# Kernel optimization log

Hardware: AMD Instinct MI355X
Metric: run time of the kernel (lower is better)

The kernel has to match this reference:

```python
import jax, jax.numpy as jnp
import numpy as np

N_HEADS = 16
MAX_CACHE_LEN = 8192
LN_EPS = 1e-5


def _layernorm(x, g, b):
    mu = jnp.mean(x, axis=-1, keepdims=True)
    var = jnp.var(x, axis=-1, keepdims=True)
    return (x - mu) * jax.lax.rsqrt(var + LN_EPS) * g + b


def setup_inputs() -> dict:
    key = jax.random.key(0)
    ks = jax.random.split(key, 8)
    b, t, d, latdim, past = 2, 2048, 2048, 512, 2048
    s = 0.02
    return {
        "x": jax.random.normal(ks[0], (b, t, d), jnp.float32),
        "latent_prev": jax.random.normal(ks[1], (b, past, latdim), jnp.float32),
        "Wq": jax.random.normal(ks[2], (d, d), jnp.float32) * s,
        "Wdown": jax.random.normal(ks[3], (d, latdim), jnp.float32) * s,
        "Wk_up": jax.random.normal(ks[4], (latdim, d), jnp.float32) * s,
        "Wv_up": jax.random.normal(ks[5], (latdim, d), jnp.float32) * s,
        "ln_g": jnp.ones((latdim,), jnp.float32),
        "ln_b": jnp.zeros((latdim,), jnp.float32),
        "Wo": jax.random.normal(ks[6], (d, d), jnp.float32) * s,
    }


def reference(x, latent_prev, Wq, Wdown, Wk_up, Wv_up, ln_g, ln_b, Wo):
    b, t, d = x.shape
    H = N_HEADS
    hd = d // H
    # q projection -> [b, t, H, hd]
    q = (x @ Wq).reshape(b, t, H, hd)
    # latent down-projection + LayerNorm, concat with cache, trim to max_cache_len
    latent_new = _layernorm(x @ Wdown, ln_g, ln_b)
    latent = jnp.concatenate([latent_prev, latent_new], axis=1)
    latent = latent[:, -MAX_CACHE_LEN:]
    S = latent.shape[1]
    past_len = min(latent_prev.shape[1], S - t)
    # up-project K/V from latent -> [b, S, H, hd]
    k = (latent @ Wk_up).reshape(b, S, H, hd)
    v = (latent @ Wv_up).reshape(b, S, H, hd)
    # offset-causal SDPA: query i attends keys j <= past_len + i
    scores = jnp.einsum("bthd,bshd->bhts", q, k) / jnp.sqrt(jnp.asarray(hd, x.dtype))
    i = jnp.arange(t)[:, None]
    j = jnp.arange(S)[None, :]
    mask = j <= (past_len + i)  # [t, S]
    scores = jnp.where(mask[None, None], scores, jnp.asarray(-1e30, scores.dtype))
    attn = jax.nn.softmax(scores, axis=-1)
    out = jnp.einsum("bhts,bshd->bthd", attn, v).reshape(b, t, d)
    return out @ Wo
```

## Files before the change

### kernel.cpp

```cpp
#include <hip/hip_runtime.h>
#include <hip/hip_bf16.h>

using bf16_t = __bf16;
typedef __bf16 bf16x8 __attribute__((ext_vector_type(8)));
typedef __bf16 bf16x4 __attribute__((ext_vector_type(4)));
typedef __bf16 bf16x2 __attribute__((ext_vector_type(2)));
typedef float  f32x4  __attribute__((ext_vector_type(4)));
typedef float  f32x16 __attribute__((ext_vector_type(16)));
typedef unsigned u32x4 __attribute__((ext_vector_type(4)));

#define MFMA16(a,b,c) __builtin_amdgcn_mfma_f32_16x16x32_bf16((a),(b),(c),0,0,0)
#define MFMA32(a,b,c) __builtin_amdgcn_mfma_f32_32x32x16_bf16((a),(b),(c),0,0,0)

__device__ __forceinline__ void load_lds16(const void* g, void* l) {
  __builtin_amdgcn_global_load_lds(
      (const __attribute__((address_space(1))) unsigned int*)g,
      (__attribute__((address_space(3))) unsigned int*)l, 16, 0, 0);
}

__device__ __forceinline__ unsigned pack_bf16(float a, float b) {
  union { bf16x2 v; unsigned u; } c;
  c.v[0] = (bf16_t)a; c.v[1] = (bf16_t)b;
  return c.u;
}

__global__ __launch_bounds__(256) void cvt_f2b(const float* __restrict__ in,
                                               bf16_t* __restrict__ out)
{
  const size_t i = ((size_t)blockIdx.x * 256 + threadIdx.x) * 4;
  f32x4 d = *(const f32x4*)(in + i);
  bf16x4 o;
#pragma unroll
  for (int j = 0; j < 4; ++j) o[j] = (bf16_t)d[j];
  *(bf16x4*)(out + i) = o;
}

__global__ __launch_bounds__(256) void cvt_transpose(const float* __restrict__ in,
                                                     bf16_t* __restrict__ out,
                                                     int R, int C)
{
  __shared__ __align__(16) bf16_t t[64 * 80];
  const int r0 = blockIdx.y * 64, c0 = blockIdx.x * 64;
  const int rr = threadIdx.x >> 4;
  const int c4 = (threadIdx.x & 15) * 4;
#pragma unroll
  for (int i = 0; i < 4; ++i) {
    const int r = rr + i * 16;
    f32x4 d = *(const f32x4*)(in + (size_t)(r0 + r) * C + c0 + c4);
#pragma unroll
    for (int j = 0; j < 4; ++j) t[(c4 + j) * 80 + r] = (bf16_t)d[j];
  }
  __syncthreads();
  const int a  = threadIdx.x >> 3;
  const int bc = (threadIdx.x & 7) * 8;
#pragma unroll
  for (int half = 0; half < 2; ++half) {
    const int cc = a + half * 32;
    bf16x8 d = *(const bf16x8*)&t[cc * 80 + bc];
    *(bf16x8*)(out + (size_t)(c0 + cc) * R + r0 + bc) = d;
  }
}

template <typename OutT>
__global__ __launch_bounds__(256) void gemm128(const bf16_t* __restrict__ A,
                                               const bf16_t* __restrict__ BT,
                                               OutT* __restrict__ C,
                                               int M, int N, int K, float scale,
                                               long long zB, long long zC)
{
  __shared__ __align__(16) bf16_t As[128 * 32];
  __shared__ __align__(16) bf16_t Bs[128 * 32];
  const int tid = threadIdx.x;
  BT += (size_t)blockIdx.z * zB;
  C  += (size_t)blockIdx.z * zC;
  const int m0 = blockIdx.y * 128, n0 = blockIdx.x * 128;
  const int lane = tid & 63, w = tid >> 6;
  const int quad = lane >> 4, l15 = lane & 15;
  const int wm = (w >> 1) * 64, wn = (w & 1) * 64;
  const int s_row = tid >> 2;
  const int g_off = ((tid & 3) ^ (s_row & 3)) * 8;
  const int quadp = (quad ^ (l15 & 3)) * 8;
  const bf16_t* Ap0 = A  + (size_t)(m0 + s_row) * K + g_off;
  const bf16_t* Ap1 = A  + (size_t)(m0 + 64 + s_row) * K + g_off;
  const bf16_t* Bp0 = BT + (size_t)(n0 + s_row) * K + g_off;
  const bf16_t* Bp1 = BT + (size_t)(n0 + 64 + s_row) * K + g_off;

  f32x4 acc[4][4] = {};

  for (int k0 = 0; k0 < K; k0 += 32) {
    __syncthreads();
    load_lds16(Ap0 + k0, As + tid * 8);
    load_lds16(Ap1 + k0, As + tid * 8 + 2048);
    load_lds16(Bp0 + k0, Bs + tid * 8);
    load_lds16(Bp1 + k0, Bs + tid * 8 + 2048);
    __syncthreads();
    bf16x8 af[4], bfr[4];
#pragma unroll
    for (int fi = 0; fi < 4; ++fi)
      af[fi] = *(const bf16x8*)&As[(wm + fi * 16 + l15) * 32 + quadp];
#pragma unroll
    for (int fj = 0; fj < 4; ++fj)
      bfr[fj] = *(const bf16x8*)&Bs[(wn + fj * 16 + l15) * 32 + quadp];
#pragma unroll
    for (int fi = 0; fi < 4; ++fi)
#pragma unroll
      for (int fj = 0; fj < 4; ++fj)
        acc[fi][fj] = MFMA16(af[fi], bfr[fj], acc[fi][fj]);
  }

#pragma unroll
  for (int fi = 0; fi < 4; ++fi)
#pragma unroll
    for (int fj = 0; fj < 4; ++fj)
#pragma unroll
      for (int r = 0; r < 4; ++r) {
        const int row = m0 + wm + fi * 16 + quad * 4 + r;
        const int col = n0 + wn + fj * 16 + l15;
        C[(size_t)row * N + col] = (OutT)(acc[fi][fj][r] * scale);
      }
}

__global__ __launch_bounds__(256) void copy_prev_f(const float* __restrict__ prev,
                                                   bf16_t* __restrict__ latent)
{
  const size_t v    = (size_t)blockIdx.x * 256 + threadIdx.x;
  const size_t flat = v * 4;
  const size_t per  = (size_t)2048 * 512;
  const size_t b    = flat / per, rem = flat % per;
  f32x4 d = *(const f32x4*)(prev + flat);
  bf16x4 o;
#pragma unroll
  for (int j = 0; j < 4; ++j) o[j] = (bf16_t)d[j];
  *(bf16x4*)(latent + b * ((size_t)4096 * 512) + rem) = o;
}

__global__ __launch_bounds__(256) void ln_kernel(const bf16_t* __restrict__ in,
                                                 const float* __restrict__ g_,
                                                 const float* __restrict__ b_,
                                                 bf16_t* __restrict__ latent)
{
  const int row = blockIdx.x;
  const int tid = threadIdx.x;
  const float x0 = (float)in[(size_t)row * 512 + tid];
  const float x1 = (float)in[(size_t)row * 512 + 256 + tid];
  float s  = x0 + x1;
  float sq = x0 * x0 + x1 * x1;
#pragma unroll
  for (int off = 1; off < 64; off <<= 1) {
    s  += __shfl_xor(s, off);
    sq += __shfl_xor(sq, off);
  }
  __shared__ float red[8];
  const int w = tid >> 6;
  if ((tid & 63) == 0) { red[w] = s; red[4 + w] = sq; }
  __syncthreads();
  s  = red[0] + red[1] + red[2] + red[3];
  sq = red[4] + red[5] + red[6] + red[7];
  const float mu   = s * (1.0f / 512.0f);
  const float var  = sq * (1.0f / 512.0f) - mu * mu;
  const float rstd = rsqrtf(var + 1e-5f);
  const int b = row >> 11, tt = row & 2047;
  bf16_t* outp = latent + ((size_t)b * 4096 + 2048 + tt) * 512;
  outp[tid]       = (bf16_t)((x0 - mu) * rstd * g_[tid]       + b_[tid]);
  outp[tid + 256] = (bf16_t)((x1 - mu) * rstd * g_[tid + 256] + b_[tid + 256]);
}

__global__ __launch_bounds__(256) void attn3(const bf16_t* __restrict__ q,
                                             const bf16_t* __restrict__ k,
                                             const bf16_t* __restrict__ vT,
                                             bf16_t* __restrict__ out)
{
  __shared__ __align__(16) bf16_t smem[32768];

  const int tid = threadIdx.x;
  const int lane = tid & 63, w = tid >> 6;
  const int l31 = lane & 31, h5 = lane >> 5;
  int qt = blockIdx.x;
  if (blockIdx.z) qt = 15 - qt;
  const int h = blockIdx.y, b = blockIdx.z;
  const int q0 = qt * 128;
  const int qg = q0 + l31 * 4 + w;

  bf16x8 qf[8];
  const bf16_t* qb = q + ((size_t)(b * 2048 + qg)) * 2048 + h * 128 + h5 * 8;
#pragma unroll
  for (int fc = 0; fc < 8; ++fc) qf[fc] = *(const bf16x8*)(qb + fc * 16);

  const bf16_t* kbase = k + ((size_t)b * 4096) * 2048 + h * 128;
  const bf16_t* vbase = vT + ((size_t)(b * 16 + h)) * 128 * 4096;

  int ks_key[4], ks_go[4], vs_feat[4], vs_go[4];
#pragma unroll
  for (int p = 0; p < 4; ++p) {
    const int slot = tid + 256 * p;
    const int key = slot >> 4, ph = slot & 15;
    ks_key[p] = key;
    ks_go[p]  = (((ph & 8) | ((ph & 7) ^ (key & 7)))) * 8;
    const int ft = slot >> 3, p2 = slot & 7;
    vs_feat[p] = ft;
    vs_go[p]   = (p2 ^ (ft & 7)) * 8;
  }
  int kfo[8], vfo[4];
#pragma unroll
  for (int fc = 0; fc < 8; ++fc) {
    const int L = fc * 2 + h5;
    kfo[fc] = l31 * 128 + ((L & 8) | ((L & 7) ^ (l31 & 7))) * 8;
  }
#pragma unroll
  for (int kc = 0; kc < 4; ++kc) {
    const int L = kc * 2 + h5;
    vfo[kc] = l31 * 64 + (L ^ (l31 & 7)) * 8;
  }

  f32x16 o[4] = {};
  float m = -1e30f, l = 0.f;
  const int send = 2048 + q0 + 128;

#pragma unroll
  for (int p = 0; p < 4; ++p) {
    load_lds16(kbase + (size_t)ks_key[p] * 2048 + ks_go[p],
               smem + (tid + 256 * p) * 8);
    load_lds16(vbase + (size_t)vs_feat[p] * 4096 + vs_go[p],
               smem + 16384 + (tid + 256 * p) * 8);
  }
  __syncthreads();

  int cur = 0;
  for (int s0 = 0; s0 < send; s0 += 64) {
    const int s1 = s0 + 64;
    if (s1 < send) {
      const int nxt = (cur ^ 1) * 8192;
#pragma unroll
      for (int p = 0; p < 4; ++p) {
        load_lds16(kbase + (size_t)(s1 + ks_key[p]) * 2048 + ks_go[p],
                   smem + nxt + (tid + 256 * p) * 8);
        load_lds16(vbase + (size_t)vs_feat[p] * 4096 + s1 + vs_go[p],
                   smem + 16384 + nxt + (tid + 256 * p) * 8);
      }
    }
    const bf16_t* Kc = smem + cur * 8192;
    const bf16_t* Vc = smem + 16384 + cur * 8192;

    f32x16 st[2] = {};
#pragma unroll
    for (int fc = 0; fc < 8; ++fc) {
      bf16x8 k0 = *(const bf16x8*)&Kc[kfo[fc]];
      bf16x8 k1 = *(const bf16x8*)&Kc[4096 + kfo[fc]];
      st[0] = MFMA32(k0, qf[fc], st[0]);
      st[1] = MFMA32(k1, qf[fc], st[1]);
    }

    if (s0 + 63 > 2048 + q0) {
#pragma unroll
      for (int t = 0; t < 2; ++t)
#pragma unroll
        for (int i = 0; i < 16; ++i) {
          const int key = s0 + 32 * t + (i & 3) + 8 * (i >> 2) + 4 * h5;
          if (key > 2048 + qg) st[t][i] = -1e30f;
        }
    }

    float mt = st[0][0];
#pragma unroll
    for (int i = 1; i < 16; ++i) mt = fmaxf(mt, st[0][i]);
#pragma unroll
    for (int i = 0; i < 16; ++i) mt = fmaxf(mt, st[1][i]);
    mt = fmaxf(mt, __shfl_xor(mt, 32));

    if (__any(mt > m)) {
      const float mnew = fmaxf(m, mt);
      const float alpha = __expf(m - mnew);
#pragma unroll
      for (int ft = 0; ft < 4; ++ft)
#pragma unroll
        for (int i = 0; i < 16; ++i) o[ft][i] *= alpha;
      l *= alpha;
      m = mnew;
    }

    float rs = 0.f;
    unsigned up[2][4][2];
#pragma unroll
    for (int t = 0; t < 2; ++t)
#pragma unroll
      for (int g = 0; g < 4; ++g) {
        const float p0 = __expf(st[t][4 * g + 0] - m);
        const float p1 = __expf(st[t][4 * g + 1] - m);
        const float p2 = __expf(st[t][4 * g + 2] - m);
        const float p3 = __expf(st[t][4 * g + 3] - m);
        rs += (p0 + p1) + (p2 + p3);
        up[t][g][0] = pack_bf16(p0, p1);
        up[t][g][1] = pack_bf16(p2, p3);
      }
    rs += __shfl_xor(rs, 32);
    l += rs;

#pragma unroll
    for (int kc = 0; kc < 4; ++kc) {
      const int t = kc >> 1, gp = (kc & 1) * 2;
      const unsigned a0 = up[t][gp][0],     a1 = up[t][gp][1];
      const unsigned b0 = up[t][gp + 1][0], b1 = up[t][gp + 1][1];
      const unsigned xa0 = __shfl_xor(a0, 32), xa1 = __shfl_xor(a1, 32);
      const unsigned xb0 = __shfl_xor(b0, 32), xb1 = __shfl_xor(b1, 32);
      u32x4 uw;
      uw[0] = h5 ? xb0 : a0;
      uw[1] = h5 ? xb1 : a1;
      uw[2] = h5 ? b0 : xa0;
      uw[3] = h5 ? b1 : xa1;
      union { u32x4 u; bf16x8 v; } pc; pc.u = uw;
      const bf16x8 pf = pc.v;
#pragma unroll
      for (int ft = 0; ft < 4; ++ft) {
        bf16x8 vf = *(const bf16x8*)&Vc[ft * 2048 + vfo[kc]];
        o[ft] = MFMA32(vf, pf, o[ft]);
      }
    }

    __syncthreads();
    cur ^= 1;
  }

  const float inv = 1.0f / l;
  const int rowp_w = w * 32 + l31;
#pragma unroll
  for (int ft = 0; ft < 4; ++ft)
#pragma unroll
    for (int g = 0; g < 4; ++g) {
      bf16x4 pk;
#pragma unroll
      for (int r = 0; r < 4; ++r) pk[r] = (bf16_t)(o[ft][4 * g + r] * inv);
      *(bf16x4*)&smem[rowp_w * 136 + ft * 32 + g * 8 + h5 * 4] = pk;
    }
  __syncthreads();
#pragma unroll
  for (int p = 0; p < 8; ++p) {
    const int c = tid + 256 * p;
    const int rowp = c >> 4, chk = c & 15;
    const int ql = (rowp & 31) * 4 + (rowp >> 5);
    bf16x8 d = *(const bf16x8*)&smem[rowp * 136 + chk * 8];
    *(bf16x8*)(out + ((size_t)(b * 2048 + q0 + ql)) * 2048 + h * 128 + chk * 8) = d;
  }
}

extern "C" void kernel_launch(void* const* d_in, const int* in_sizes, int n_in,
                              void* d_out, int out_size, void* d_ws, size_t ws_size,
                              hipStream_t stream)
{
  (void)in_sizes; (void)n_in; (void)out_size; (void)ws_size;
  const float* x        = (const float*)d_in[0];
  const float* lat_prev = (const float*)d_in[1];
  const float* Wq       = (const float*)d_in[2];
  const float* Wdown    = (const float*)d_in[3];
  const float* Wk_up    = (const float*)d_in[4];
  const float* Wv_up    = (const float*)d_in[5];
  const float* ln_g     = (const float*)d_in[6];
  const float* ln_b     = (const float*)d_in[7];
  const float* Wo       = (const float*)d_in[8];
  float* out = (float*)d_out;

  char* p = (char*)d_ws;
  auto alloc = [&](size_t elems) { bf16_t* r = (bf16_t*)p; p += elems * 2; return r; };
  bf16_t* xb     = alloc((size_t)4096 * 2048);
  bf16_t* WqT    = alloc((size_t)2048 * 2048);
  bf16_t* WdT    = alloc((size_t)512 * 2048);
  bf16_t* qbuf   = alloc((size_t)4096 * 2048);
  bf16_t* latpre = alloc((size_t)4096 * 512);
  bf16_t* latent = alloc((size_t)2 * 4096 * 512);
  bf16_t* kbuf   = alloc((size_t)8192 * 2048);
  bf16_t* vTb    = alloc((size_t)2 * 2048 * 4096);
  bf16_t* aout   = alloc((size_t)4096 * 2048);
  bf16_t* WoT  = xb;
  bf16_t* WkT  = latpre;
  bf16_t* WvT  = latpre + (size_t)2048 * 512;

  const dim3 B(256);
  const float qscale = 0.08838834764831845f;

  cvt_f2b<<<dim3(8192), B, 0, stream>>>(x, xb);
  cvt_transpose<<<dim3(32, 32), B, 0, stream>>>(Wq,    WqT, 2048, 2048);
  cvt_transpose<<<dim3(8,  32), B, 0, stream>>>(Wdown, WdT, 2048, 512);
  gemm128<bf16_t><<<dim3(16, 32), B, 0, stream>>>(xb, WqT, qbuf, 4096, 2048, 2048, qscale, 0, 0);
  gemm128<bf16_t><<<dim3(4,  32), B, 0, stream>>>(xb, WdT, latpre, 4096, 512, 2048, 1.0f, 0, 0);
  copy_prev_f<<<dim3(2048), B, 0, stream>>>(lat_prev, latent);
  ln_kernel<<<dim3(4096), B, 0, stream>>>(latpre, ln_g, ln_b, latent);
  cvt_transpose<<<dim3(32, 32), B, 0, stream>>>(Wo,    WoT, 2048, 2048);
  cvt_transpose<<<dim3(32, 8),  B, 0, stream>>>(Wk_up, WkT, 512, 2048);
  cvt_transpose<<<dim3(32, 8),  B, 0, stream>>>(Wv_up, WvT, 512, 2048);
  gemm128<bf16_t><<<dim3(16, 64), B, 0, stream>>>(latent, WkT, kbuf, 8192, 2048, 512, 1.0f, 0, 0);
  gemm128<bf16_t><<<dim3(32, 16, 2), B, 0, stream>>>(WvT, latent, vTb, 2048, 4096, 512, 1.0f,
                                                     (long long)4096 * 512,
                                                     (long long)2048 * 4096);
  attn3<<<dim3(16, 16, 2), B, 0, stream>>>(qbuf, kbuf, vTb, aout);
  gemm128<float><<<dim3(16, 32), B, 0, stream>>>(aout, WoT, out, 4096, 2048, 2048, 1.0f, 0, 0);
}
```

Before: 588.5 us.

## Load K and V fragments directly from global memory in attention kernel

Removes the double-buffered LDS staging of K and V tiles in the attention kernel. Each wave now reads its MFMA operand fragments straight from global memory (served by L2/L1) and keeps V fragments in registers, which eliminates the per-iteration __syncthreads. Each of the four waves in a block now fetches the same K/V data separately, so global/cache traffic and register pressure go up and prefetch overlap across iterations is lost.

Measured after the change: 771.2 us. +31.0%, slower.

```diff
diff --git a/kernel.cpp b/kernel.cpp
--- a/kernel.cpp
+++ b/kernel.cpp
@@ -165,12 +165,12 @@
   outp[tid + 256] = (bf16_t)((x1 - mu) * rstd * g_[tid + 256] + b_[tid + 256]);
 }
 
-__global__ __launch_bounds__(256) void attn3(const bf16_t* __restrict__ q,
+__global__ __launch_bounds__(256) void attn4(const bf16_t* __restrict__ q,
                                              const bf16_t* __restrict__ k,
                                              const bf16_t* __restrict__ vT,
                                              bf16_t* __restrict__ out)
 {
-  __shared__ __align__(16) bf16_t smem[32768];
+  __shared__ __align__(16) bf16_t Ot[128 * 136];
 
   const int tid = threadIdx.x;
   const int lane = tid & 63, w = tid >> 6;
@@ -186,69 +186,29 @@
 #pragma unroll
   for (int fc = 0; fc < 8; ++fc) qf[fc] = *(const bf16x8*)(qb + fc * 16);
 
-  const bf16_t* kbase = k + ((size_t)b * 4096) * 2048 + h * 128;
-  const bf16_t* vbase = vT + ((size_t)(b * 16 + h)) * 128 * 4096;
-
-  int ks_key[4], ks_go[4], vs_feat[4], vs_go[4];
-#pragma unroll
-  for (int p = 0; p < 4; ++p) {
-    const int slot = tid + 256 * p;
-    const int key = slot >> 4, ph = slot & 15;
-    ks_key[p] = key;
-    ks_go[p]  = (((ph & 8) | ((ph & 7) ^ (key & 7)))) * 8;
-    const int ft = slot >> 3, p2 = slot & 7;
-    vs_feat[p] = ft;
-    vs_go[p]   = (p2 ^ (ft & 7)) * 8;
-  }
-  int kfo[8], vfo[4];
-#pragma unroll
-  for (int fc = 0; fc < 8; ++fc) {
-    const int L = fc * 2 + h5;
-    kfo[fc] = l31 * 128 + ((L & 8) | ((L & 7) ^ (l31 & 7))) * 8;
-  }
-#pragma unroll
-  for (int kc = 0; kc < 4; ++kc) {
-    const int L = kc * 2 + h5;
-    vfo[kc] = l31 * 64 + (L ^ (l31 & 7)) * 8;
-  }
+  const bf16_t* kb = k + ((size_t)(b * 4096 + l31)) * 2048 + h * 128 + h5 * 8;
+  const bf16_t* vb = vT + ((size_t)(b * 16 + h) * 128 + l31) * 4096 + h5 * 8;
 
   f32x16 o[4] = {};
   float m = -1e30f, l = 0.f;
   const int send = 2048 + q0 + 128;
 
-#pragma unroll
-  for (int p = 0; p < 4; ++p) {
-    load_lds16(kbase + (size_t)ks_key[p] * 2048 + ks_go[p],
-               smem + (tid + 256 * p) * 8);
-    load_lds16(vbase + (size_t)vs_feat[p] * 4096 + vs_go[p],
-               smem + 16384 + (tid + 256 * p) * 8);
-  }
-  __syncthreads();
-
-  int cur = 0;
   for (int s0 = 0; s0 < send; s0 += 64) {
-    const int s1 = s0 + 64;
-    if (s1 < send) {
-      const int nxt = (cur ^ 1) * 8192;
-#pragma unroll
-      for (int p = 0; p < 4; ++p) {
-        load_lds16(kbase + (size_t)(s1 + ks_key[p]) * 2048 + ks_go[p],
-                   smem + nxt + (tid + 256 * p) * 8);
-        load_lds16(vbase + (size_t)vs_feat[p] * 4096 + s1 + vs_go[p],
-                   smem + 16384 + nxt + (tid + 256 * p) * 8);
-      }
-    }
-    const bf16_t* Kc = smem + cur * 8192;
-    const bf16_t* Vc = smem + 16384 + cur * 8192;
-
     f32x16 st[2] = {};
 #pragma unroll
     for (int fc = 0; fc < 8; ++fc) {
-      bf16x8 k0 = *(const bf16x8*)&Kc[kfo[fc]];
-      bf16x8 k1 = *(const bf16x8*)&Kc[4096 + kfo[fc]];
+      bf16x8 k0 = *(const bf16x8*)(kb + (size_t)s0 * 2048 + fc * 16);
+      bf16x8 k1 = *(const bf16x8*)(kb + (size_t)(s0 + 32) * 2048 + fc * 16);
       st[0] = MFMA32(k0, qf[fc], st[0]);
       st[1] = MFMA32(k1, qf[fc], st[1]);
     }
+
+    bf16x8 vf[4][4];
+#pragma unroll
+    for (int kc = 0; kc < 4; ++kc)
+#pragma unroll
+      for (int ft = 0; ft < 4; ++ft)
+        vf[kc][ft] = *(const bf16x8*)(vb + (size_t)(ft * 32) * 4096 + s0 + kc * 16);
 
     if (s0 + 63 > 2048 + q0) {
 #pragma unroll
@@ -310,14 +270,9 @@
       union { u32x4 u; bf16x8 v; } pc; pc.u = uw;
       const bf16x8 pf = pc.v;
 #pragma unroll
-      for (int ft = 0; ft < 4; ++ft) {
-        bf16x8 vf = *(const bf16x8*)&Vc[ft * 2048 + vfo[kc]];
-        o[ft] = MFMA32(vf, pf, o[ft]);
-      }
-    }
-
-    __syncthreads();
-    cur ^= 1;
+      for (int ft = 0; ft < 4; ++ft)
+        o[ft] = MFMA32(vf[kc][ft], pf, o[ft]);
+    }
   }
 
   const float inv = 1.0f / l;
@@ -329,7 +284,7 @@
       bf16x4 pk;
 #pragma unroll
       for (int r = 0; r < 4; ++r) pk[r] = (bf16_t)(o[ft][4 * g + r] * inv);
-      *(bf16x4*)&smem[rowp_w * 136 + ft * 32 + g * 8 + h5 * 4] = pk;
+      *(bf16x4*)&Ot[rowp_w * 136 + ft * 32 + g * 8 + h5 * 4] = pk;
     }
   __syncthreads();
 #pragma unroll
@@ -337,7 +292,7 @@
     const int c = tid + 256 * p;
     const int rowp = c >> 4, chk = c & 15;
     const int ql = (rowp & 31) * 4 + (rowp >> 5);
-    bf16x8 d = *(const bf16x8*)&smem[rowp * 136 + chk * 8];
+    bf16x8 d = *(const bf16x8*)&Ot[rowp * 136 + chk * 8];
     *(bf16x8*)(out + ((size_t)(b * 2048 + q0 + ql)) * 2048 + h * 128 + chk * 8) = d;
   }
 }
@@ -390,6 +345,6 @@
   gemm128<bf16_t><<<dim3(32, 16, 2), B, 0, stream>>>(WvT, latent, vTb, 2048, 4096, 512, 1.0f,
                                                      (long long)4096 * 512,
                                                      (long long)2048 * 4096);
-  attn3<<<dim3(16, 16, 2), B, 0, stream>>>(qbuf, kbuf, vTb, aout);
+  attn4<<<dim3(16, 16, 2), B, 0, stream>>>(qbuf, kbuf, vTb, aout);
   gemm128<float><<<dim3(16, 32), B, 0, stream>>>(aout, WoT, out, 4096, 2048, 2048, 1.0f, 0, 0);
 }
```
